# Kernel optimization log

Hardware: AMD Instinct MI355X
Metric: run time of the kernel (lower is better)

The kernel has to match this reference:

```python
import jax, jax.numpy as jnp
import numpy as np

# Dims: B batch, CK key dim, CV value dim, NOBJ objects, T memory frames, HxW feature map
B, CK, CV, NOBJ, T, H, W = 1, 64, 512, 2, 2, 64, 64


def setup_inputs() -> dict:
    key = jax.random.key(0)
    k1, k2, k3, k4, k5 = jax.random.split(key, 5)
    return {
        "query_key": jax.random.normal(k1, (B, CK, H, W), jnp.float32),
        "query_selection": jax.random.uniform(k2, (B, CK, H, W), jnp.float32),
        "memory_key": jax.random.normal(k3, (B, CK, T, H, W), jnp.float32),
        "memory_shrinkage": jax.random.uniform(k4, (B, 1, T, H, W), jnp.float32),
        "memory_value": jax.random.normal(k5, (B, NOBJ, CV, T, H, W), jnp.float32),
    }


def reference(query_key, query_selection, memory_key, memory_shrinkage, memory_value):
    b, nobj, cv = memory_value.shape[:3]
    ck = memory_key.shape[1]
    h, w = query_key.shape[-2:]
    hw = h * w
    mk = memory_key.reshape(b, ck, -1)            # (b, ck, N) with N = T*H*W
    ms = memory_shrinkage.reshape(b, -1)          # (b, N)
    qk = query_key.reshape(b, ck, hw)             # (b, ck, hw)
    qe = query_selection.reshape(b, ck, hw)       # (b, ck, hw)
    mv = memory_value.reshape(b, nobj * cv, -1)   # (b, nobj*cv, N)

    # Negative L2 similarity with selection weighting (XMem get_similarity)
    a_sq = jnp.einsum('bcn,bcp->bnp', mk * mk, qe)            # (b, N, hw)
    two_ab = 2.0 * jnp.einsum('bcn,bcp->bnp', mk, qk * qe)    # (b, N, hw)
    b_sq = jnp.sum(qe * qk * qk, axis=1, keepdims=True)       # (b, 1, hw)
    inv_sqrt_ck = np.float32(1.0 / np.sqrt(ck))
    sim = (two_ab - a_sq - b_sq) * ms[:, :, None] * inv_sqrt_ck

    # Softmax over memory slots (dim N), then weighted readout
    aff = jax.nn.softmax(sim, axis=1)                          # (b, N, hw)
    mem = jnp.einsum('bvn,bnp->bvp', mv, aff)                  # (b, nobj*cv, hw)
    return mem.reshape(b, nobj, cv, h, w)
```

## Files before the change

kernel.cpp:

```cpp
#include <hip/hip_runtime.h>
#include <stdint.h>

typedef unsigned short u16;
typedef __attribute__((ext_vector_type(4))) float f32x4;
typedef __attribute__((ext_vector_type(8))) __bf16 bf16x8;
typedef __attribute__((ext_vector_type(4))) unsigned int u32x4;

#define HWPX 4096
#define NMEM 8192
#define CKD  64
#define VROWS 1024

__device__ __forceinline__ u16 f2bf(float x) {
    union { float f; unsigned u; } v; v.f = x;
    unsigned r = v.u + 0x7FFFu + ((v.u >> 16) & 1u);
    return (u16)(r >> 16);
}

__device__ __forceinline__ void gld_lds16(const void* g, void* l) {
    __builtin_amdgcn_global_load_lds(
        (const __attribute__((address_space(1))) uint32_t*)g,
        (__attribute__((address_space(3))) uint32_t*)l, 16, 0, 0);
}

__global__ void prep_all(const float* __restrict__ qk, const float* __restrict__ qe,
                         const float* __restrict__ mk, const float* __restrict__ mv,
                         u16* __restrict__ Qhat, float* __restrict__ bsq,
                         u16* __restrict__ Khat, u16* __restrict__ mvb,
                         float* __restrict__ outz) {
    const int bx = blockIdx.x;
    const int tid = threadIdx.x;
    if (bx < 16) {
        int p = bx * 256 + tid;
        float acc = 0.f;
        #pragma unroll 4
        for (int c = 0; c < CKD; ++c) {
            float k = qk[c * HWPX + p];
            float e = qe[c * HWPX + p];
            Qhat[p * 128 + c]      = f2bf(k * e);
            Qhat[p * 128 + 64 + c] = f2bf(e);
            acc += e * k * k;
        }
        bsq[p] = acc;
    } else if (bx < 48) {
        int n = (bx - 16) * 256 + tid;
        #pragma unroll 4
        for (int c = 0; c < CKD; ++c) {
            float m = mk[c * NMEM + n];
            Khat[n * 128 + c]      = f2bf(2.f * m);
            Khat[n * 128 + 64 + c] = f2bf(-m * m);
        }
    } else if (bx < 48 + 8192) {
        int i = (bx - 48) * 256 + tid;
        float4 v = ((const float4*)mv)[i];
        u16 o0 = f2bf(v.x), o1 = f2bf(v.y), o2 = f2bf(v.z), o3 = f2bf(v.w);
        unsigned lo = (unsigned)o0 | ((unsigned)o1 << 16);
        unsigned hi = (unsigned)o2 | ((unsigned)o3 << 16);
        ((uint2*)mvb)[i] = make_uint2(lo, hi);
    } else {
        int i = (bx - 48 - 8192) * 256 + tid;
        ((float4*)outz)[i] = make_float4(0.f, 0.f, 0.f, 0.f);
    }
}

__launch_bounds__(256, 4)
__global__ void gemm1_kernel(const u16* __restrict__ Qhat, const u16* __restrict__ Khat,
                             const float* __restrict__ bsq, const float* __restrict__ ms,
                             u16* __restrict__ Pt, float* __restrict__ dpart) {
    __shared__ __align__(16) u16 smem[17408];
    u16* Qs = smem;
    u16* Ks = smem + 8192;

    const int tid  = threadIdx.x;
    const int l    = tid & 63;
    const int w    = tid >> 6;
    const int quad = l >> 4;
    const int l15  = l & 15;
    const int wm = w >> 1, wn = w & 1;
    const int p0 = blockIdx.x * 128;
    const int n0 = blockIdx.y * 128;

    const int rsub = tid >> 3;
    const int csw  = (tid & 7) ^ (rsub & 7);

    f32x4 acc[4][4] = {};

    #pragma unroll
    for (int h = 0; h < 2; ++h) {
        if (h) __syncthreads();
        #pragma unroll
        for (int rnd = 0; rnd < 4; ++rnd) {
            gld_lds16(Qhat + (size_t)(p0 + rnd * 32 + rsub) * 128 + h * 64 + csw * 8,
                      Qs + rnd * 2048 + w * 512);
            gld_lds16(Khat + (size_t)(n0 + rnd * 32 + rsub) * 128 + h * 64 + csw * 8,
                      Ks + rnd * 2048 + w * 512);
        }
        __syncthreads();
        #pragma unroll
        for (int kk = 0; kk < 2; ++kk) {
            bf16x8 a[4], b[4];
            #pragma unroll
            for (int mi = 0; mi < 4; ++mi) {
                int row = wm * 64 + mi * 16 + l15;
                a[mi] = *(const bf16x8*)(Qs + row * 64 + (((kk * 4 + quad) ^ (l15 & 7)) << 3));
            }
            #pragma unroll
            for (int ni = 0; ni < 4; ++ni) {
                int row = wn * 64 + ni * 16 + l15;
                b[ni] = *(const bf16x8*)(Ks + row * 64 + (((kk * 4 + quad) ^ (l15 & 7)) << 3));
            }
            #pragma unroll
            for (int mi = 0; mi < 4; ++mi)
                #pragma unroll
                for (int ni = 0; ni < 4; ++ni)
                    acc[mi][ni] = __builtin_amdgcn_mfma_f32_16x16x32_bf16(a[mi], b[ni], acc[mi][ni], 0, 0, 0);
        }
    }

    float msv[4];
    #pragma unroll
    for (int ni = 0; ni < 4; ++ni)
        msv[ni] = ms[n0 + wn * 64 + ni * 16 + l15] * 0.125f;
    float bsv[4][4];
    #pragma unroll
    for (int mi = 0; mi < 4; ++mi)
        #pragma unroll
        for (int r = 0; r < 4; ++r)
            bsv[mi][r] = bsq[p0 + wm * 64 + mi * 16 + quad * 4 + r];

    __syncthreads();
    u16* Ps = smem;
    float rowsum[4][4] = {};
    #pragma unroll
    for (int mi = 0; mi < 4; ++mi) {
        #pragma unroll
        for (int ni = 0; ni < 4; ++ni) {
            f32x4 v = acc[mi][ni];
            int col = wn * 64 + ni * 16 + l15;
            #pragma unroll
            for (int r = 0; r < 4; ++r) {
                int rowl = wm * 64 + mi * 16 + quad * 4 + r;
                float pv = __expf((v[r] - bsv[mi][r]) * msv[ni]);
                rowsum[mi][r] += pv;
                Ps[rowl * 136 + col] = f2bf(pv);
            }
        }
    }
    #pragma unroll
    for (int mi = 0; mi < 4; ++mi)
        #pragma unroll
        for (int r = 0; r < 4; ++r) {
            float s = rowsum[mi][r];
            s += __shfl_xor(s, 1);
            s += __shfl_xor(s, 2);
            s += __shfl_xor(s, 4);
            s += __shfl_xor(s, 8);
            rowsum[mi][r] = s;
        }
    {
        float myv = 0.f;
        #pragma unroll
        for (int mi = 0; mi < 4; ++mi)
            #pragma unroll
            for (int r = 0; r < 4; ++r)
                if (l15 == mi * 4 + r) myv = rowsum[mi][r];
        int slice = blockIdx.y * 2 + wn;
        dpart[(size_t)slice * HWPX + p0 + wm * 64 + (l15 >> 2) * 16 + quad * 4 + (l15 & 3)] = myv;
    }
    __syncthreads();

    {
        const size_t tileOff = ((size_t)blockIdx.x * 64 + blockIdx.y) * 16384;
        #pragma unroll
        for (int i = 0; i < 8; ++i) {
            int row = i * 16 + (tid >> 4);
            const u32x4* src = (const u32x4*)(Ps + row * 136 + (tid & 15) * 8);
            u32x4* dst = (u32x4*)(Pt + tileOff + i * 2048 + tid * 8);
            *dst = *src;
        }
    }
}

__launch_bounds__(256, 4)
__global__ void gemm2_kernel(const u16* __restrict__ Ab, const u16* __restrict__ Bt,
                             const float* __restrict__ dpart, float* __restrict__ outacc) {
    __shared__ __align__(16) u16 As[128 * 64];
    __shared__ __align__(16) u16 Bs[128 * 64];

    const int tid  = threadIdx.x;
    const int l    = tid & 63;
    const int w    = tid >> 6;
    const int quad = l >> 4;
    const int l15  = l & 15;
    const int wm = w >> 1, wn = w & 1;

    const int lin = blockIdx.x + (blockIdx.y << 3) + (blockIdx.z << 8);
    const int vb  = (lin >> 3) & 7;
    const int pb  = (lin & 7) | (((lin >> 6) & 3) << 3);
    const int kz  = lin >> 8;
    const int v0 = vb * 128;
    const int p0 = pb * 128;
    const int kbeg = kz * (NMEM / 4);
    const int kend = kbeg + (NMEM / 4);

    const int rsub = tid >> 3;
    const int csw  = (tid & 7) ^ (rsub & 7);

    f32x4 acc[4][4] = {};

    for (int k0 = kbeg; k0 < kend; k0 += 64) {
        const int nb = k0 >> 7;
        const int nh = (k0 >> 6) & 1;
        const u16* bsrc = Bt + ((size_t)pb * 64 + nb) * 16384 + nh * 64;
        __syncthreads();
        #pragma unroll
        for (int rnd = 0; rnd < 4; ++rnd) {
            gld_lds16(Ab + (size_t)(v0 + rnd * 32 + rsub) * NMEM + k0 + csw * 8,
                      As + rnd * 2048 + w * 512);
            gld_lds16(bsrc + (rnd * 32 + rsub) * 128 + csw * 8,
                      Bs + rnd * 2048 + w * 512);
        }
        __syncthreads();
        #pragma unroll
        for (int kk = 0; kk < 2; ++kk) {
            bf16x8 a[4], b[4];
            #pragma unroll
            for (int mi = 0; mi < 4; ++mi) {
                int row = wm * 64 + mi * 16 + l15;
                a[mi] = *(const bf16x8*)(As + row * 64 + (((kk * 4 + quad) ^ (l15 & 7)) << 3));
            }
            #pragma unroll
            for (int ni = 0; ni < 4; ++ni) {
                int row = wn * 64 + ni * 16 + l15;
                b[ni] = *(const bf16x8*)(Bs + row * 64 + (((kk * 4 + quad) ^ (l15 & 7)) << 3));
            }
            #pragma unroll
            for (int mi = 0; mi < 4; ++mi)
                #pragma unroll
                for (int ni = 0; ni < 4; ++ni)
                    acc[mi][ni] = __builtin_amdgcn_mfma_f32_16x16x32_bf16(a[mi], b[ni], acc[mi][ni], 0, 0, 0);
        }
    }

    __syncthreads();
    float* dtmp = (float*)As;
    float* dinvs = (float*)Bs;
    {
        int p = tid & 127, h = tid >> 7;
        float s = 0.f;
        #pragma unroll 8
        for (int sl = 0; sl < 64; ++sl)
            s += dpart[(size_t)(h * 64 + sl) * HWPX + p0 + p];
        dtmp[tid] = s;
    }
    __syncthreads();
    if (tid < 128) dinvs[tid] = 1.0f / (dtmp[tid] + dtmp[tid + 128]);
    __syncthreads();

    float dinv[4];
    #pragma unroll
    for (int ni = 0; ni < 4; ++ni)
        dinv[ni] = dinvs[wn * 64 + ni * 16 + l15];

    #pragma unroll
    for (int mi = 0; mi < 4; ++mi) {
        #pragma unroll
        for (int ni = 0; ni < 4; ++ni) {
            int col = p0 + wn * 64 + ni * 16 + l15;
            f32x4 v = acc[mi][ni];
            #pragma unroll
            for (int r = 0; r < 4; ++r) {
                int row = v0 + wm * 64 + mi * 16 + quad * 4 + r;
                atomicAdd(&outacc[(size_t)row * HWPX + col], v[r] * dinv[ni]);
            }
        }
    }
}

extern "C" void kernel_launch(void* const* d_in, const int* in_sizes, int n_in,
                              void* d_out, int out_size, void* d_ws, size_t ws_size,
                              hipStream_t stream) {
    const float* qk = (const float*)d_in[0];
    const float* qe = (const float*)d_in[1];
    const float* mk = (const float*)d_in[2];
    const float* ms = (const float*)d_in[3];
    const float* mv = (const float*)d_in[4];
    float* out = (float*)d_out;

    char* ws = (char*)d_ws;
    u16*   Pt    = (u16*)ws;
    u16*   mvb   = (u16*)(ws + ((size_t)64 << 20));
    u16*   Khat  = (u16*)(ws + ((size_t)80 << 20));
    u16*   Qhat  = (u16*)(ws + ((size_t)82 << 20));
    float* bsq   = (float*)(ws + ((size_t)83 << 20));
    float* dpart = (float*)(ws + ((size_t)83 << 20) + 65536);

    prep_all<<<48 + 8192 + 4096, 256, 0, stream>>>(qk, qe, mk, mv, Qhat, bsq, Khat, mvb, out);

    dim3 g1(HWPX / 128, NMEM / 128);
    gemm1_kernel<<<g1, 256, 0, stream>>>(Qhat, Khat, bsq, ms, Pt, dpart);

    dim3 g2(8, 32, 4);
    gemm2_kernel<<<g2, 256, 0, stream>>>(mvb, Pt, dpart, out);
}
```

Before: 231.8 us.

## Fuse prep and both GEMMs into one persistent kernel with grid barriers

Replaces three kernel launches with a single persistent kernel of 1024 blocks that loops over the prep work, runs a software grid barrier, computes the GEMM1 tiles (two per block), runs a second barrier, then does GEMM2. This removes launch gaps and inter-kernel drains. In exchange it relies on all 1024 blocks being co-resident, since otherwise the spin barrier deadlocks. The barrier counters are never reset between calls and rely on an odd wraparound check (value minus NBLK equal to zero or 0xAAAAAAAA), which looks fragile across repeated launches.

```diff
diff --git a/kernel.cpp b/kernel.cpp
--- a/kernel.cpp
+++ b/kernel.cpp
@@ -10,6 +10,7 @@
 #define NMEM 8192
 #define CKD  64
 #define VROWS 1024
+#define NBLK 1024
 
 __device__ __forceinline__ u16 f2bf(float x) {
     union { float f; unsigned u; } v; v.f = x;
@@ -23,255 +24,272 @@
         (__attribute__((address_space(3))) uint32_t*)l, 16, 0, 0);
 }
 
-__global__ void prep_all(const float* __restrict__ qk, const float* __restrict__ qe,
-                         const float* __restrict__ mk, const float* __restrict__ mv,
-                         u16* __restrict__ Qhat, float* __restrict__ bsq,
-                         u16* __restrict__ Khat, u16* __restrict__ mvb,
-                         float* __restrict__ outz) {
-    const int bx = blockIdx.x;
+__device__ __forceinline__ void gridbar(unsigned* c) {
+    __syncthreads();
+    if (threadIdx.x == 0) {
+        __threadfence();
+        atomicAdd(c, 1u);
+        for (;;) {
+            unsigned v = __hip_atomic_load(c, __ATOMIC_RELAXED, __HIP_MEMORY_SCOPE_AGENT);
+            unsigned d = v - (unsigned)NBLK;
+            if (d == 0u || d == 0xAAAAAAAAu) break;
+            __builtin_amdgcn_s_sleep(2);
+        }
+        __threadfence();
+    }
+    __syncthreads();
+}
+
+__global__ __launch_bounds__(256, 4)
+void xmem_mega(const float* __restrict__ qk, const float* __restrict__ qe,
+               const float* __restrict__ mk, const float* __restrict__ ms,
+               const float* __restrict__ mv, float* __restrict__ out,
+               u16* __restrict__ Qhat, float* __restrict__ bsq,
+               u16* __restrict__ Khat, u16* __restrict__ mvb,
+               u16* __restrict__ Pt, float* __restrict__ dpart,
+               unsigned* __restrict__ c0, unsigned* __restrict__ c1) {
+    __shared__ __align__(16) u16 smem[17408];
+
+    const int blk = blockIdx.x;
     const int tid = threadIdx.x;
-    if (bx < 16) {
-        int p = bx * 256 + tid;
-        float acc = 0.f;
-        #pragma unroll 4
-        for (int c = 0; c < CKD; ++c) {
-            float k = qk[c * HWPX + p];
-            float e = qe[c * HWPX + p];
-            Qhat[p * 128 + c]      = f2bf(k * e);
-            Qhat[p * 128 + 64 + c] = f2bf(e);
-            acc += e * k * k;
-        }
-        bsq[p] = acc;
-    } else if (bx < 48) {
-        int n = (bx - 16) * 256 + tid;
-        #pragma unroll 4
-        for (int c = 0; c < CKD; ++c) {
-            float m = mk[c * NMEM + n];
-            Khat[n * 128 + c]      = f2bf(2.f * m);
-            Khat[n * 128 + 64 + c] = f2bf(-m * m);
-        }
-    } else if (bx < 48 + 8192) {
-        int i = (bx - 48) * 256 + tid;
-        float4 v = ((const float4*)mv)[i];
-        u16 o0 = f2bf(v.x), o1 = f2bf(v.y), o2 = f2bf(v.z), o3 = f2bf(v.w);
-        unsigned lo = (unsigned)o0 | ((unsigned)o1 << 16);
-        unsigned hi = (unsigned)o2 | ((unsigned)o3 << 16);
-        ((uint2*)mvb)[i] = make_uint2(lo, hi);
-    } else {
-        int i = (bx - 48 - 8192) * 256 + tid;
-        ((float4*)outz)[i] = make_float4(0.f, 0.f, 0.f, 0.f);
-    }
-}
-
-__launch_bounds__(256, 4)
-__global__ void gemm1_kernel(const u16* __restrict__ Qhat, const u16* __restrict__ Khat,
-                             const float* __restrict__ bsq, const float* __restrict__ ms,
-                             u16* __restrict__ Pt, float* __restrict__ dpart) {
-    __shared__ __align__(16) u16 smem[17408];
-    u16* Qs = smem;
-    u16* Ks = smem + 8192;
-
-    const int tid  = threadIdx.x;
     const int l    = tid & 63;
     const int w    = tid >> 6;
     const int quad = l >> 4;
     const int l15  = l & 15;
     const int wm = w >> 1, wn = w & 1;
-    const int p0 = blockIdx.x * 128;
-    const int n0 = blockIdx.y * 128;
-
-    const int rsub = tid >> 3;
-    const int csw  = (tid & 7) ^ (rsub & 7);
-
-    f32x4 acc[4][4] = {};
-
-    #pragma unroll
-    for (int h = 0; h < 2; ++h) {
-        if (h) __syncthreads();
-        #pragma unroll
-        for (int rnd = 0; rnd < 4; ++rnd) {
-            gld_lds16(Qhat + (size_t)(p0 + rnd * 32 + rsub) * 128 + h * 64 + csw * 8,
-                      Qs + rnd * 2048 + w * 512);
-            gld_lds16(Khat + (size_t)(n0 + rnd * 32 + rsub) * 128 + h * 64 + csw * 8,
-                      Ks + rnd * 2048 + w * 512);
-        }
-        __syncthreads();
-        #pragma unroll
-        for (int kk = 0; kk < 2; ++kk) {
-            bf16x8 a[4], b[4];
-            #pragma unroll
-            for (int mi = 0; mi < 4; ++mi) {
-                int row = wm * 64 + mi * 16 + l15;
-                a[mi] = *(const bf16x8*)(Qs + row * 64 + (((kk * 4 + quad) ^ (l15 & 7)) << 3));
-            }
+
+    for (int u = blk; u < 48 + 8192 + 4096; u += NBLK) {
+        if (u < 16) {
+            int p = u * 256 + tid;
+            float acc = 0.f;
+            #pragma unroll 4
+            for (int c = 0; c < CKD; ++c) {
+                float k = qk[c * HWPX + p];
+                float e = qe[c * HWPX + p];
+                Qhat[p * 128 + c]      = f2bf(k * e);
+                Qhat[p * 128 + 64 + c] = f2bf(e);
+                acc += e * k * k;
+            }
+            bsq[p] = acc;
+        } else if (u < 48) {
+            int n = (u - 16) * 256 + tid;
+            #pragma unroll 4
+            for (int c = 0; c < CKD; ++c) {
+                float m = mk[c * NMEM + n];
+                Khat[n * 128 + c]      = f2bf(2.f * m);
+                Khat[n * 128 + 64 + c] = f2bf(-m * m);
+            }
+        } else if (u < 48 + 8192) {
+            int i = (u - 48) * 256 + tid;
+            float4 v = ((const float4*)mv)[i];
+            u16 o0 = f2bf(v.x), o1 = f2bf(v.y), o2 = f2bf(v.z), o3 = f2bf(v.w);
+            unsigned lo = (unsigned)o0 | ((unsigned)o1 << 16);
+            unsigned hi = (unsigned)o2 | ((unsigned)o3 << 16);
+            ((uint2*)mvb)[i] = make_uint2(lo, hi);
+        } else {
+            int i = (u - 48 - 8192) * 256 + tid;
+            ((float4*)out)[i] = make_float4(0.f, 0.f, 0.f, 0.f);
+        }
+    }
+
+    gridbar(c0);
+
+    for (int it = 0; it < 2; ++it) {
+        const int tile = blk + it * NBLK;
+        const int bx = tile & 31;
+        const int by = tile >> 5;
+        const int p0 = bx * 128;
+        const int n0 = by * 128;
+
+        u16* Qs = smem;
+        u16* Ks = smem + 8192;
+
+        const int rsub = tid >> 3;
+        const int csw  = (tid & 7) ^ (rsub & 7);
+
+        f32x4 acc[4][4] = {};
+
+        #pragma unroll
+        for (int h = 0; h < 2; ++h) {
+            __syncthreads();
+            #pragma unroll
+            for (int rnd = 0; rnd < 4; ++rnd) {
+                gld_lds16(Qhat + (size_t)(p0 + rnd * 32 + rsub) * 128 + h * 64 + csw * 8,
+                          Qs + rnd * 2048 + w * 512);
+                gld_lds16(Khat + (size_t)(n0 + rnd * 32 + rsub) * 128 + h * 64 + csw * 8,
+                          Ks + rnd * 2048 + w * 512);
+            }
+            __syncthreads();
+            #pragma unroll
+            for (int kk = 0; kk < 2; ++kk) {
+                bf16x8 a[4], b[4];
+                #pragma unroll
+                for (int mi = 0; mi < 4; ++mi) {
+                    int row = wm * 64 + mi * 16 + l15;
+                    a[mi] = *(const bf16x8*)(Qs + row * 64 + (((kk * 4 + quad) ^ (l15 & 7)) << 3));
+                }
+                #pragma unroll
+                for (int ni = 0; ni < 4; ++ni) {
+                    int row = wn * 64 + ni * 16 + l15;
+                    b[ni] = *(const bf16x8*)(Ks + row * 64 + (((kk * 4 + quad) ^ (l15 & 7)) << 3));
+                }
+                #pragma unroll
+                for (int mi = 0; mi < 4; ++mi)
+                    #pragma unroll
+                    for (int ni = 0; ni < 4; ++ni)
+                        acc[mi][ni] = __builtin_amdgcn_mfma_f32_16x16x32_bf16(a[mi], b[ni], acc[mi][ni], 0, 0, 0);
+            }
+        }
+
+        float msv[4];
+        #pragma unroll
+        for (int ni = 0; ni < 4; ++ni)
+            msv[ni] = ms[n0 + wn * 64 + ni * 16 + l15] * 0.125f;
+        float bsv[4][4];
+        #pragma unroll
+        for (int mi = 0; mi < 4; ++mi)
+            #pragma unroll
+            for (int r = 0; r < 4; ++r)
+                bsv[mi][r] = bsq[p0 + wm * 64 + mi * 16 + quad * 4 + r];
+
+        __syncthreads();
+        u16* Ps = smem;
+        float rowsum[4][4] = {};
+        #pragma unroll
+        for (int mi = 0; mi < 4; ++mi) {
             #pragma unroll
             for (int ni = 0; ni < 4; ++ni) {
-                int row = wn * 64 + ni * 16 + l15;
-                b[ni] = *(const bf16x8*)(Ks + row * 64 + (((kk * 4 + quad) ^ (l15 & 7)) << 3));
-            }
+                f32x4 v = acc[mi][ni];
+                int col = wn * 64 + ni * 16 + l15;
+                #pragma unroll
+                for (int r = 0; r < 4; ++r) {
+                    int rowl = wm * 64 + mi * 16 + quad * 4 + r;
+                    float pv = __expf((v[r] - bsv[mi][r]) * msv[ni]);
+                    rowsum[mi][r] += pv;
+                    Ps[rowl * 136 + col] = f2bf(pv);
+                }
+            }
+        }
+        #pragma unroll
+        for (int mi = 0; mi < 4; ++mi)
+            #pragma unroll
+            for (int r = 0; r < 4; ++r) {
+                float s = rowsum[mi][r];
+                s += __shfl_xor(s, 1);
+                s += __shfl_xor(s, 2);
+                s += __shfl_xor(s, 4);
+                s += __shfl_xor(s, 8);
+                rowsum[mi][r] = s;
+            }
+        {
+            float myv = 0.f;
             #pragma unroll
             for (int mi = 0; mi < 4; ++mi)
                 #pragma unroll
-                for (int ni = 0; ni < 4; ++ni)
-                    acc[mi][ni] = __builtin_amdgcn_mfma_f32_16x16x32_bf16(a[mi], b[ni], acc[mi][ni], 0, 0, 0);
+                for (int r = 0; r < 4; ++r)
+                    if (l15 == mi * 4 + r) myv = rowsum[mi][r];
+            int slice = by * 2 + wn;
+            dpart[(size_t)slice * HWPX + p0 + wm * 64 + (l15 >> 2) * 16 + quad * 4 + (l15 & 3)] = myv;
+        }
+        __syncthreads();
+
+        {
+            const size_t tileOff = ((size_t)bx * 64 + by) * 16384;
+            #pragma unroll
+            for (int i = 0; i < 8; ++i) {
+                int row = i * 16 + (tid >> 4);
+                const u32x4* src = (const u32x4*)(Ps + row * 136 + (tid & 15) * 8);
+                u32x4* dst = (u32x4*)(Pt + tileOff + i * 2048 + tid * 8);
+                *dst = *src;
+            }
         }
     }
 
-    float msv[4];
-    #pragma unroll
-    for (int ni = 0; ni < 4; ++ni)
-        msv[ni] = ms[n0 + wn * 64 + ni * 16 + l15] * 0.125f;
-    float bsv[4][4];
-    #pragma unroll
-    for (int mi = 0; mi < 4; ++mi)
-        #pragma unroll
-        for (int r = 0; r < 4; ++r)
-            bsv[mi][r] = bsq[p0 + wm * 64 + mi * 16 + quad * 4 + r];
-
-    __syncthreads();
-    u16* Ps = smem;
-    float rowsum[4][4] = {};
-    #pragma unroll
-    for (int mi = 0; mi < 4; ++mi) {
-        #pragma unroll
-        for (int ni = 0; ni < 4; ++ni) {
-            f32x4 v = acc[mi][ni];
-            int col = wn * 64 + ni * 16 + l15;
-            #pragma unroll
-            for (int r = 0; r < 4; ++r) {
-                int rowl = wm * 64 + mi * 16 + quad * 4 + r;
-                float pv = __expf((v[r] - bsv[mi][r]) * msv[ni]);
-                rowsum[mi][r] += pv;
-                Ps[rowl * 136 + col] = f2bf(pv);
-            }
-        }
-    }
-    #pragma unroll
-    for (int mi = 0; mi < 4; ++mi)
-        #pragma unroll
-        for (int r = 0; r < 4; ++r) {
-            float s = rowsum[mi][r];
-            s += __shfl_xor(s, 1);
-            s += __shfl_xor(s, 2);
-            s += __shfl_xor(s, 4);
-            s += __shfl_xor(s, 8);
-            rowsum[mi][r] = s;
-        }
+    gridbar(c1);
+
     {
-        float myv = 0.f;
-        #pragma unroll
-        for (int mi = 0; mi < 4; ++mi)
-            #pragma unroll
-            for (int r = 0; r < 4; ++r)
-                if (l15 == mi * 4 + r) myv = rowsum[mi][r];
-        int slice = blockIdx.y * 2 + wn;
-        dpart[(size_t)slice * HWPX + p0 + wm * 64 + (l15 >> 2) * 16 + quad * 4 + (l15 & 3)] = myv;
-    }
-    __syncthreads();
-
-    {
-        const size_t tileOff = ((size_t)blockIdx.x * 64 + blockIdx.y) * 16384;
-        #pragma unroll
-        for (int i = 0; i < 8; ++i) {
-            int row = i * 16 + (tid >> 4);
-            const u32x4* src = (const u32x4*)(Ps + row * 136 + (tid & 15) * 8);
-            u32x4* dst = (u32x4*)(Pt + tileOff + i * 2048 + tid * 8);
-            *dst = *src;
-        }
-    }
-}
-
-__launch_bounds__(256, 4)
-__global__ void gemm2_kernel(const u16* __restrict__ Ab, const u16* __restrict__ Bt,
-                             const float* __restrict__ dpart, float* __restrict__ outacc) {
-    __shared__ __align__(16) u16 As[128 * 64];
-    __shared__ __align__(16) u16 Bs[128 * 64];
-
-    const int tid  = threadIdx.x;
-    const int l    = tid & 63;
-    const int w    = tid >> 6;
-    const int quad = l >> 4;
-    const int l15  = l & 15;
-    const int wm = w >> 1, wn = w & 1;
-
-    const int lin = blockIdx.x + (blockIdx.y << 3) + (blockIdx.z << 8);
-    const int vb  = (lin >> 3) & 7;
-    const int pb  = (lin & 7) | (((lin >> 6) & 3) << 3);
-    const int kz  = lin >> 8;
-    const int v0 = vb * 128;
-    const int p0 = pb * 128;
-    const int kbeg = kz * (NMEM / 4);
-    const int kend = kbeg + (NMEM / 4);
-
-    const int rsub = tid >> 3;
-    const int csw  = (tid & 7) ^ (rsub & 7);
-
-    f32x4 acc[4][4] = {};
-
-    for (int k0 = kbeg; k0 < kend; k0 += 64) {
-        const int nb = k0 >> 7;
-        const int nh = (k0 >> 6) & 1;
-        const u16* bsrc = Bt + ((size_t)pb * 64 + nb) * 16384 + nh * 64;
-        __syncthreads();
-        #pragma unroll
-        for (int rnd = 0; rnd < 4; ++rnd) {
-            gld_lds16(Ab + (size_t)(v0 + rnd * 32 + rsub) * NMEM + k0 + csw * 8,
-                      As + rnd * 2048 + w * 512);
-            gld_lds16(bsrc + (rnd * 32 + rsub) * 128 + csw * 8,
-                      Bs + rnd * 2048 + w * 512);
-        }
-        __syncthreads();
-        #pragma unroll
-        for (int kk = 0; kk < 2; ++kk) {
-            bf16x8 a[4], b[4];
-            #pragma unroll
-            for (int mi = 0; mi < 4; ++mi) {
-                int row = wm * 64 + mi * 16 + l15;
-                a[mi] = *(const bf16x8*)(As + row * 64 + (((kk * 4 + quad) ^ (l15 & 7)) << 3));
-            }
+        u16* As = smem;
+        u16* Bs = smem + 8192;
+
+        const int lin = blk;
+        const int vb  = (lin >> 3) & 7;
+        const int pb  = (lin & 7) | (((lin >> 6) & 3) << 3);
+        const int kz  = lin >> 8;
+        const int v0 = vb * 128;
+        const int p0 = pb * 128;
+        const int kbeg = kz * (NMEM / 4);
+        const int kend = kbeg + (NMEM / 4);
+
+        const int rsub = tid >> 3;
+        const int csw  = (tid & 7) ^ (rsub & 7);
+
+        f32x4 acc[4][4] = {};
+
+        for (int k0 = kbeg; k0 < kend; k0 += 64) {
+            const int nb = k0 >> 7;
+            const int nh = (k0 >> 6) & 1;
+            const u16* bsrc = Pt + ((size_t)pb * 64 + nb) * 16384 + nh * 64;
+            __syncthreads();
+            #pragma unroll
+            for (int rnd = 0; rnd < 4; ++rnd) {
+                gld_lds16(mvb + (size_t)(v0 + rnd * 32 + rsub) * NMEM + k0 + csw * 8,
+                          As + rnd * 2048 + w * 512);
+                gld_lds16(bsrc + (rnd * 32 + rsub) * 128 + csw * 8,
+                          Bs + rnd * 2048 + w * 512);
+            }
+            __syncthreads();
+            #pragma unroll
+            for (int kk = 0; kk < 2; ++kk) {
+                bf16x8 a[4], b[4];
+                #pragma unroll
+                for (int mi = 0; mi < 4; ++mi) {
+                    int row = wm * 64 + mi * 16 + l15;
+                    a[mi] = *(const bf16x8*)(As + row * 64 + (((kk * 4 + quad) ^ (l15 & 7)) << 3));
+                }
+                #pragma unroll
+                for (int ni = 0; ni < 4; ++ni) {
+                    int row = wn * 64 + ni * 16 + l15;
+                    b[ni] = *(const bf16x8*)(Bs + row * 64 + (((kk * 4 + quad) ^ (l15 & 7)) << 3));
+                }
+                #pragma unroll
+                for (int mi = 0; mi < 4; ++mi)
+                    #pragma unroll
+                    for (int ni = 0; ni < 4; ++ni)
+                        acc[mi][ni] = __builtin_amdgcn_mfma_f32_16x16x32_bf16(a[mi], b[ni], acc[mi][ni], 0, 0, 0);
+            }
+        }
+
+        __syncthreads();
+        float* dtmp = (float*)As;
+        float* dinvs = (float*)Bs;
+        {
+            int p = tid & 127, h = tid >> 7;
+            float s = 0.f;
+            #pragma unroll 8
+            for (int sl = 0; sl < 64; ++sl)
+                s += dpart[(size_t)(h * 64 + sl) * HWPX + p0 + p];
+            dtmp[tid] = s;
+        }
+        __syncthreads();
+        if (tid < 128) dinvs[tid] = 1.0f / (dtmp[tid] + dtmp[tid + 128]);
+        __syncthreads();
+
+        float dinv[4];
+        #pragma unroll
+        for (int ni = 0; ni < 4; ++ni)
+            dinv[ni] = dinvs[wn * 64 + ni * 16 + l15];
+
+        #pragma unroll
+        for (int mi = 0; mi < 4; ++mi) {
             #pragma unroll
             for (int ni = 0; ni < 4; ++ni) {
-                int row = wn * 64 + ni * 16 + l15;
-                b[ni] = *(const bf16x8*)(Bs + row * 64 + (((kk * 4 + quad) ^ (l15 & 7)) << 3));
-            }
-            #pragma unroll
-            for (int mi = 0; mi < 4; ++mi)
-                #pragma unroll
-                for (int ni = 0; ni < 4; ++ni)
-                    acc[mi][ni] = __builtin_amdgcn_mfma_f32_16x16x32_bf16(a[mi], b[ni], acc[mi][ni], 0, 0, 0);
-        }
-    }
-
-    __syncthreads();
-    float* dtmp = (float*)As;
-    float* dinvs = (float*)Bs;
-    {
-        int p = tid & 127, h = tid >> 7;
-        float s = 0.f;
-        #pragma unroll 8
-        for (int sl = 0; sl < 64; ++sl)
-            s += dpart[(size_t)(h * 64 + sl) * HWPX + p0 + p];
-        dtmp[tid] = s;
-    }
-    __syncthreads();
-    if (tid < 128) dinvs[tid] = 1.0f / (dtmp[tid] + dtmp[tid + 128]);
-    __syncthreads();
-
-    float dinv[4];
-    #pragma unroll
-    for (int ni = 0; ni < 4; ++ni)
-        dinv[ni] = dinvs[wn * 64 + ni * 16 + l15];
-
-    #pragma unroll
-    for (int mi = 0; mi < 4; ++mi) {
-        #pragma unroll
-        for (int ni = 0; ni < 4; ++ni) {
-            int col = p0 + wn * 64 + ni * 16 + l15;
-            f32x4 v = acc[mi][ni];
-            #pragma unroll
-            for (int r = 0; r < 4; ++r) {
-                int row = v0 + wm * 64 + mi * 16 + quad * 4 + r;
-                atomicAdd(&outacc[(size_t)row * HWPX + col], v[r] * dinv[ni]);
+                int col = p0 + wn * 64 + ni * 16 + l15;
+                f32x4 v = acc[mi][ni];
+                #pragma unroll
+                for (int r = 0; r < 4; ++r) {
+                    int row = v0 + wm * 64 + mi * 16 + quad * 4 + r;
+                    atomicAdd(&out[(size_t)row * HWPX + col], v[r] * dinv[ni]);
+                }
             }
         }
     }
@@ -293,13 +311,10 @@
     u16*   Khat  = (u16*)(ws + ((size_t)80 << 20));
     u16*   Qhat  = (u16*)(ws + ((size_t)82 << 20));
     float* bsq   = (float*)(ws + ((size_t)83 << 20));
+    unsigned* c0 = (unsigned*)(ws + ((size_t)83 << 20) + 32768);
+    unsigned* c1 = c0 + 16;
     float* dpart = (float*)(ws + ((size_t)83 << 20) + 65536);
 
-    prep_all<<<48 + 8192 + 4096, 256, 0, stream>>>(qk, qe, mk, mv, Qhat, bsq, Khat, mvb, out);
-
-    dim3 g1(HWPX / 128, NMEM / 128);
-    gemm1_kernel<<<g1, 256, 0, stream>>>(Qhat, Khat, bsq, ms, Pt, dpart);
-
-    dim3 g2(8, 32, 4);
-    gemm2_kernel<<<g2, 256, 0, stream>>>(mvb, Pt, dpart, out);
-}
+    xmem_mega<<<NBLK, 256, 0, stream>>>(qk, qe, mk, ms, mv, out,
+                                        Qhat, bsq, Khat, mvb, Pt, dpart, c0, c1);
+}
```

Result: slower. 495.0 us (+113.5%).

## Overlap value bf16 conversion and output zeroing with the similarity GEMM

Applied to the files above, without the earlier changes.

Moves the memory_value fp32-to-bf16 conversion and the output zero-fill out of the prep kernel and into extra leading blocks of the first GEMM launch. The prep kernel now only builds the query and key operands, so it becomes tiny. The bandwidth-bound conversion can then run at the same time as the compute-bound GEMM tiles instead of before them. The conversion blocks each process 16 float4s per thread, and GEMM tile indices are now derived from a flattened 1D block index.

```diff
diff --git a/kernel.cpp b/kernel.cpp
--- a/kernel.cpp
+++ b/kernel.cpp
@@ -23,11 +23,10 @@
         (__attribute__((address_space(3))) uint32_t*)l, 16, 0, 0);
 }
 
-__global__ void prep_all(const float* __restrict__ qk, const float* __restrict__ qe,
-                         const float* __restrict__ mk, const float* __restrict__ mv,
-                         u16* __restrict__ Qhat, float* __restrict__ bsq,
-                         u16* __restrict__ Khat, u16* __restrict__ mvb,
-                         float* __restrict__ outz) {
+__global__ void prep_qk(const float* __restrict__ qk, const float* __restrict__ qe,
+                        const float* __restrict__ mk,
+                        u16* __restrict__ Qhat, float* __restrict__ bsq,
+                        u16* __restrict__ Khat) {
     const int bx = blockIdx.x;
     const int tid = threadIdx.x;
     if (bx < 16) {
@@ -42,7 +41,7 @@
             acc += e * k * k;
         }
         bsq[p] = acc;
-    } else if (bx < 48) {
+    } else {
         int n = (bx - 16) * 256 + tid;
         #pragma unroll 4
         for (int c = 0; c < CKD; ++c) {
@@ -50,35 +49,54 @@
             Khat[n * 128 + c]      = f2bf(2.f * m);
             Khat[n * 128 + 64 + c] = f2bf(-m * m);
         }
-    } else if (bx < 48 + 8192) {
-        int i = (bx - 48) * 256 + tid;
-        float4 v = ((const float4*)mv)[i];
-        u16 o0 = f2bf(v.x), o1 = f2bf(v.y), o2 = f2bf(v.z), o3 = f2bf(v.w);
-        unsigned lo = (unsigned)o0 | ((unsigned)o1 << 16);
-        unsigned hi = (unsigned)o2 | ((unsigned)o3 << 16);
-        ((uint2*)mvb)[i] = make_uint2(lo, hi);
-    } else {
-        int i = (bx - 48 - 8192) * 256 + tid;
-        ((float4*)outz)[i] = make_float4(0.f, 0.f, 0.f, 0.f);
     }
 }
 
 __launch_bounds__(256, 4)
-__global__ void gemm1_kernel(const u16* __restrict__ Qhat, const u16* __restrict__ Khat,
-                             const float* __restrict__ bsq, const float* __restrict__ ms,
-                             u16* __restrict__ Pt, float* __restrict__ dpart) {
+__global__ void gemm1_combo(const u16* __restrict__ Qhat, const u16* __restrict__ Khat,
+                            const float* __restrict__ bsq, const float* __restrict__ ms,
+                            const float* __restrict__ mv,
+                            u16* __restrict__ Pt, float* __restrict__ dpart,
+                            u16* __restrict__ mvb, float* __restrict__ outz) {
+    const int blk = blockIdx.x;
+    const int tid = threadIdx.x;
+
+    if (blk < 512) {
+        #pragma unroll 4
+        for (int it = 0; it < 16; ++it) {
+            int i = blk * 4096 + it * 256 + tid;
+            float4 v = ((const float4*)mv)[i];
+            u16 o0 = f2bf(v.x), o1 = f2bf(v.y), o2 = f2bf(v.z), o3 = f2bf(v.w);
+            unsigned lo = (unsigned)o0 | ((unsigned)o1 << 16);
+            unsigned hi = (unsigned)o2 | ((unsigned)o3 << 16);
+            ((uint2*)mvb)[i] = make_uint2(lo, hi);
+        }
+        return;
+    }
+    if (blk < 768) {
+        #pragma unroll 4
+        for (int it = 0; it < 16; ++it) {
+            int i = (blk - 512) * 4096 + it * 256 + tid;
+            ((float4*)outz)[i] = make_float4(0.f, 0.f, 0.f, 0.f);
+        }
+        return;
+    }
+
     __shared__ __align__(16) u16 smem[17408];
     u16* Qs = smem;
     u16* Ks = smem + 8192;
 
-    const int tid  = threadIdx.x;
+    const int tile = blk - 768;
+    const int bx = tile & 31;
+    const int by = tile >> 5;
+    const int p0 = bx * 128;
+    const int n0 = by * 128;
+
     const int l    = tid & 63;
     const int w    = tid >> 6;
     const int quad = l >> 4;
     const int l15  = l & 15;
     const int wm = w >> 1, wn = w & 1;
-    const int p0 = blockIdx.x * 128;
-    const int n0 = blockIdx.y * 128;
 
     const int rsub = tid >> 3;
     const int csw  = (tid & 7) ^ (rsub & 7);
@@ -164,13 +182,13 @@
             #pragma unroll
             for (int r = 0; r < 4; ++r)
                 if (l15 == mi * 4 + r) myv = rowsum[mi][r];
-        int slice = blockIdx.y * 2 + wn;
+        int slice = by * 2 + wn;
         dpart[(size_t)slice * HWPX + p0 + wm * 64 + (l15 >> 2) * 16 + quad * 4 + (l15 & 3)] = myv;
     }
     __syncthreads();
 
     {
-        const size_t tileOff = ((size_t)blockIdx.x * 64 + blockIdx.y) * 16384;
+        const size_t tileOff = ((size_t)bx * 64 + by) * 16384;
         #pragma unroll
         for (int i = 0; i < 8; ++i) {
             int row = i * 16 + (tid >> 4);
@@ -295,10 +313,9 @@
     float* bsq   = (float*)(ws + ((size_t)83 << 20));
     float* dpart = (float*)(ws + ((size_t)83 << 20) + 65536);
 
-    prep_all<<<48 + 8192 + 4096, 256, 0, stream>>>(qk, qe, mk, mv, Qhat, bsq, Khat, mvb, out);
-
-    dim3 g1(HWPX / 128, NMEM / 128);
-    gemm1_kernel<<<g1, 256, 0, stream>>>(Qhat, Khat, bsq, ms, Pt, dpart);
+    prep_qk<<<48, 256, 0, stream>>>(qk, qe, mk, Qhat, bsq, Khat);
+
+    gemm1_combo<<<2816, 256, 0, stream>>>(Qhat, Khat, bsq, ms, mv, Pt, dpart, mvb, out);
 
     dim3 g2(8, 32, 4);
     gemm2_kernel<<<g2, 256, 0, stream>>>(mvb, Pt, dpart, out);
```

Measured after the change: 228.9 us. Within noise of the previous version (-1.3%).
